# Kernel optimization log

Measured on AMD Instinct MI355X. Metric: run time of the kernel, lower is better.

The kernel has to match this reference:

```python
import jax, jax.numpy as jnp
import numpy as np

EPS = 1e-9


def setup_inputs() -> dict:
    key = jax.random.key(0)
    kE, kQ, kK, kV = jax.random.split(key, 4)
    B, S, D = 8, 2048, 256
    return {
        "E": jax.random.normal(kE, (B, S, D), dtype=jnp.float32),
        "WQ": jax.random.normal(kQ, (D, D), dtype=jnp.float32) * (1.0 / np.sqrt(D)),
        "WK": jax.random.normal(kK, (D, D), dtype=jnp.float32) * (1.0 / np.sqrt(D)),
        "WV": jax.random.normal(kV, (D, D), dtype=jnp.float32) * (1.0 / np.sqrt(D)),
    }


def reference(E, WQ, WK, WV):
    # E: [B, S, D]; WQ/WK/WV: [D, D] (torch Linear weight, applied as x @ W.T)
    D = E.shape[-1]
    scale = jnp.asarray(np.sqrt(D), dtype=E.dtype)
    Q = jnp.einsum('bsd,ed->bse', E, WQ)
    K = jnp.einsum('bsd,ed->bse', E, WK)
    V = jnp.einsum('bsd,ed->bse', E, WV)
    # Full score matrix [B, S, S] (non-flash, as in the original)
    W = jnp.einsum('bqd,bkd->bqk', Q, K) / scale
    # mask=True path: causal tril mask, additionally zeroed where W == 0 exactly
    S_len = W.shape[-1]
    tril = jnp.tril(jnp.ones((S_len, S_len), dtype=W.dtype))  # [S, S]
    M = jnp.where(W == 0, jnp.zeros_like(W), tril[None, :, :])
    # custom masked softmax with epsilon denominator
    x_max = jnp.max(W, axis=-1, keepdims=True)
    x_exp = jnp.exp(W - x_max) * M
    A = x_exp / (jnp.sum(x_exp, axis=-1, keepdims=True) + EPS)
    return jnp.einsum('bqk,bkd->bqd', A, V)
```

## Files before the change

kernel.cpp:

```cpp
#include <hip/hip_runtime.h>
#include <hip/hip_bf16.h>
#include <stdint.h>


typedef __attribute__((ext_vector_type(8)))  short bf16x8;
typedef __attribute__((ext_vector_type(4)))  float f32x4;
typedef __attribute__((ext_vector_type(16))) float f32x16;
typedef __attribute__((ext_vector_type(4)))  unsigned int u32x4;

#define NEGF  -3.0e38f
#define MINIT -1.0e30f

__device__ __forceinline__ unsigned short f2bf(float f){
  union { float f; unsigned u; } v; v.f = f;
  unsigned r = v.u + 0x7FFFu + ((v.u >> 16) & 1u);
  return (unsigned short)(r >> 16);
}
__device__ __forceinline__ unsigned pk2(float a, float b){
  return (unsigned)f2bf(a) | ((unsigned)f2bf(b) << 16);
}
__device__ __forceinline__ unsigned short f2bf_n(float f){
  __hip_bfloat16 h = __float2bfloat16(f);
  return *reinterpret_cast<unsigned short*>(&h);
}
__device__ __forceinline__ unsigned pk2_n(float a, float b){
  return (unsigned)f2bf_n(a) | ((unsigned)f2bf_n(b) << 16);
}
__device__ __forceinline__ float bf2f(unsigned short h){
  union { unsigned u; float f; } v; v.u = ((unsigned)h) << 16; return v.f;
}

__global__ void wconv_kernel(const float* __restrict__ WQ, const float* __restrict__ WK,
                             const float* __restrict__ WV, unsigned short* __restrict__ Wb)
{
  const int widx = blockIdx.x, kk = blockIdx.y, n = threadIdx.x;
  const float* W = (widx==0) ? WQ : ((widx==1) ? WK : WV);
  unsigned short* dst = Wb + (size_t)widx*65536 + kk*8192 + n*32;
#pragma unroll
  for (int gp=0; gp<4; ++gp){
    const int g = gp ^ (n & 3);
    const float* src = W + (size_t)n*256 + kk*32 + g*8;
    float4 a = *reinterpret_cast<const float4*>(src);
    float4 c = *reinterpret_cast<const float4*>(src + 4);
    uint4 v; v.x = pk2(a.x,a.y); v.y = pk2(a.z,a.w); v.z = pk2(c.x,c.y); v.w = pk2(c.z,c.w);
    *reinterpret_cast<uint4*>(dst + gp*8) = v;
  }
}

__global__ __launch_bounds__(256, 3) void qkv_proj_kernel(
    const float* __restrict__ E, const unsigned short* __restrict__ Wb,
    unsigned short* __restrict__ Qb, unsigned short* __restrict__ Ka,
    unsigned short* __restrict__ Vf)
{
  __shared__ unsigned short As[32*256];
  __shared__ unsigned short Bs[2][8192];

  const int m0 = blockIdx.x * 32;
  const int b  = m0 >> 11;
  const int sb = m0 & 2047;
  const int t = threadIdx.x, lane = t & 63, w = t >> 6;
  const int hi = lane >> 4, lo = lane & 15;

  auto stageB = [&](int widx, int kk, int buf){
    const char* src = (const char*)Wb + widx*131072 + kk*16384;
    char* dst = (char*)Bs[buf];
#pragma unroll
    for (int c=0;c<4;c++){
      const int off = c*4096 + t*16;
      __builtin_amdgcn_global_load_lds(
        (const __attribute__((address_space(1))) unsigned int*)(src + off),
        (__attribute__((address_space(3))) unsigned int*)(dst + off), 16, 0, 0);
    }
  };

  stageB(0, 0, 0);
  {
    const int r = t >> 3, c0 = (t & 7) * 32;
    const float* ga = E + (size_t)(m0 + r)*256 + c0;
#pragma unroll
    for (int gg=0; gg<4; ++gg){
      float4 x = *reinterpret_cast<const float4*>(ga + gg*8);
      float4 y = *reinterpret_cast<const float4*>(ga + gg*8 + 4);
      uint4 v; v.x = pk2(x.x,x.y); v.y = pk2(x.z,x.w); v.z = pk2(y.x,y.y); v.w = pk2(y.z,y.w);
      const int g = (t & 7)*4 + gg;
      *reinterpret_cast<uint4*>((char*)As + r*512 + ((g ^ (r & 7)) << 4)) = v;
    }
  }

  const f32x4 fzero = {0.f,0.f,0.f,0.f};
  const int u = sb >> 5;
  for (int widx=0; widx<3; ++widx){
    f32x4 acc[2][4];
#pragma unroll
    for (int mi=0;mi<2;mi++)
#pragma unroll
      for (int f=0;f<4;f++) acc[mi][f] = fzero;
    if (widx) stageB(widx, 0, 0);

    for (int kk=0; kk<8; ++kk){
      const int bb = kk & 1;
      if (kk < 7) stageB(widx, kk+1, bb^1);
      if (kk < 7) asm volatile("s_waitcnt vmcnt(4) lgkmcnt(0)" ::: "memory");
      else        asm volatile("s_waitcnt vmcnt(0) lgkmcnt(0)" ::: "memory");
      __builtin_amdgcn_sched_barrier(0);
      __builtin_amdgcn_s_barrier();
      __builtin_amdgcn_sched_barrier(0);

      bf16x8 afr[2], bfr[4];
#pragma unroll
      for (int mi=0;mi<2;mi++){
        const int r = mi*16 + lo;
        afr[mi] = *reinterpret_cast<const bf16x8*>(
            (const char*)As + r*512 + (((kk*4 + hi) ^ (r & 7)) << 4));
      }
#pragma unroll
      for (int f=0;f<4;f++){
        const int n = w*64 + f*16 + lo;
        bfr[f] = *reinterpret_cast<const bf16x8*>(
            (const char*)Bs[bb] + n*64 + ((hi ^ (n & 3)) << 4));
      }
#pragma unroll
      for (int mi=0;mi<2;mi++)
#pragma unroll
        for (int f=0;f<4;f++)
          acc[mi][f] = __builtin_amdgcn_mfma_f32_16x16x32_bf16(afr[mi], bfr[f], acc[mi][f], 0,0,0);

      asm volatile("s_waitcnt lgkmcnt(0)" ::: "memory");
      __builtin_amdgcn_sched_barrier(0);
      __builtin_amdgcn_s_barrier();
    }

    if (widx == 0){
#pragma unroll
      for (int mi=0;mi<2;mi++)
#pragma unroll
        for (int f=0;f<4;f++){
          const int col = w*64 + f*16 + lo;
#pragma unroll
          for (int r=0;r<4;r++)
            Qb[(size_t)(m0 + mi*16 + hi*4 + r)*256 + col] = f2bf(acc[mi][f][r]*0.0625f);
        }
    } else if (widx == 1){
      unsigned short* Kab = Ka + (size_t)b*524288 + (size_t)u*8192;
#pragma unroll
      for (int mi=0;mi<2;mi++)
#pragma unroll
        for (int f=0;f<4;f++){
          const int c = w*4 + f;
          const int j = lo & 7;
          const int lb = 32*(lo>>3) + mi*16 + hi*4;
#pragma unroll
          for (int r=0;r<4;r++)
            Kab[(size_t)(c*64 + lb + r)*8 + j] = f2bf(acc[mi][f][r]);
        }
    } else {
      unsigned short* Vfb = Vf + (size_t)b*524288;
#pragma unroll
      for (int mi=0;mi<2;mi++)
#pragma unroll
        for (int f=0;f<4;f++){
          const int d  = w*64 + f*16 + lo;
          const int dt = d >> 5;
          const int l  = 32*(hi&1) + (d&31);
          const int j0 = 4*(hi>>1);
          unsigned short* vp = Vfb + ((size_t)((u*2 + mi)*8 + dt)*64 + l)*8 + j0;
          uint2 pw; pw.x = pk2(acc[mi][f][0], acc[mi][f][1]);
          pw.y = pk2(acc[mi][f][2], acc[mi][f][3]);
          *reinterpret_cast<uint2*>(vp) = pw;
        }
    }
  }
}

__global__ __launch_bounds__(256, 2) void attn_kernel(
    const unsigned short* __restrict__ Qb, const unsigned short* __restrict__ Ka,
    const unsigned short* __restrict__ Vf, float* __restrict__ Out,
    const int sched, unsigned short* __restrict__ Pb, float* __restrict__ ML)
{
  __shared__ char Lds[2][32768];

  const int bid  = blockIdx.x;
  const int b    = bid & 7;
  const int slot = bid >> 3;
  int tau, chunk, mode, u0, u1;
  if (sched){
    const int ts = slot >> 1; chunk = slot & 1;
    tau = (ts < 16) ? (31 - ts) : (ts - 16);
    u0 = chunk ? (tau + 1) : 0;
    u1 = chunk ? (2*tau + 2) : (tau + 1);
    mode = 1 + chunk;
  } else {
    tau = 31 - slot; chunk = 0; u0 = 0; u1 = 2*tau + 2; mode = 0;
  }
  const int Qbase = tau * 64;

  const int t = threadIdx.x;
  const int lane = t & 63, w = t >> 6;
  const int qs = w >> 1, dh = w & 1;
  const int l31 = lane & 31, h5 = lane >> 5;
  const int q_l = Qbase + qs*32 + l31;
  const int diagu = 2*tau + qs;

  const char* Kab = (const char*)Ka + (size_t)b*1048576;
  const char* Vfb = (const char*)Vf + (size_t)b*1048576;

  auto stage = [&](int uu, int buf){
    const char* gk = Kab + (size_t)uu*16384;
    const char* gv = Vfb + (size_t)uu*16384;
    char* lk = Lds[buf];
    char* lv = Lds[buf] + 16384;
#pragma unroll
    for (int i=0;i<4;i++){
      const int off = i*4096 + t*16;
      __builtin_amdgcn_global_load_lds(
        (const __attribute__((address_space(1))) unsigned int*)(gk + off),
        (__attribute__((address_space(3))) unsigned int*)(lk + off), 16, 0, 0);
      __builtin_amdgcn_global_load_lds(
        (const __attribute__((address_space(1))) unsigned int*)(gv + off),
        (__attribute__((address_space(3))) unsigned int*)(lv + off), 16, 0, 0);
    }
  };

  bf16x8 qf[16];
  {
    const unsigned short* Qp = Qb + ((size_t)(b*2048 + q_l))*256 + h5*8;
#pragma unroll
    for (int c=0;c<16;c++) qf[c] = *reinterpret_cast<const bf16x8*>(Qp + c*16);
  }

  const f32x16 z16 = {0.f,0.f,0.f,0.f,0.f,0.f,0.f,0.f,0.f,0.f,0.f,0.f,0.f,0.f,0.f,0.f};
  f32x16 accO[4];
#pragma unroll
  for (int i=0;i<4;i++) accO[i] = z16;
  float m_run = MINIT, l_run = 0.f;

  stage(u0, 0);
  if (u0 + 1 < u1) stage(u0 + 1, 1);

  for (int u = u0; u < u1; ++u){
    const int buf = (u - u0) & 1;
    if (u + 1 < u1) asm volatile("s_waitcnt vmcnt(8)" ::: "memory");
    else            asm volatile("s_waitcnt vmcnt(0)" ::: "memory");
    __builtin_amdgcn_sched_barrier(0);
    __builtin_amdgcn_s_barrier();
    __builtin_amdgcn_sched_barrier(0);

    const char* kt = Lds[buf];
    const char* lv = Lds[buf] + 16384 + dh*4096 + lane*16;

    f32x16 sv0 = z16, sv1 = z16;
#pragma unroll
    for (int c=0;c<16;c+=2){
      bf16x8 a0 = *reinterpret_cast<const bf16x8*>(kt + c*1024 + lane*16);
      bf16x8 a1 = *reinterpret_cast<const bf16x8*>(kt + (c+1)*1024 + lane*16);
      sv0 = __builtin_amdgcn_mfma_f32_32x32x16_bf16(a0, qf[c],   sv0, 0,0,0);
      sv1 = __builtin_amdgcn_mfma_f32_32x32x16_bf16(a1, qf[c+1], sv1, 0,0,0);
    }
    f32x16 s16 = sv0 + sv1;

    bf16x8 vf0[4], vf1[4];
#pragma unroll
    for (int i=0;i<4;i++){
      vf0[i] = *reinterpret_cast<const bf16x8*>(lv + i*1024);
      vf1[i] = *reinterpret_cast<const bf16x8*>(lv + 8192 + i*1024);
    }

    if (u >= diagu){
      const int kvb = u*32 + 4*h5;
#pragma unroll
      for (int r=0;r<16;r++){
        const int kv = kvb + (r&3) + 8*(r>>2);
        if (kv > q_l) s16[r] = NEGF;
      }
    }

    float t8[8], t4[4];
#pragma unroll
    for (int i=0;i<8;i++) t8[i] = fmaxf(s16[i], s16[i+8]);
#pragma unroll
    for (int i=0;i<4;i++) t4[i] = fmaxf(t8[i], t8[i+4]);
    float pmax = fmaxf(fmaxf(t4[0],t4[1]), fmaxf(t4[2],t4[3]));
    pmax = fmaxf(pmax, __shfl_xor(pmax, 32, 64));

    if (!__all(pmax - m_run <= 8.0f)){
      const float mn = fmaxf(m_run, pmax);
      const float alpha = __expf(m_run - mn);
#pragma unroll
      for (int i=0;i<4;i++) accO[i] *= alpha;
      l_run *= alpha;
      m_run = mn;
    }
    float p[16];
#pragma unroll
    for (int r=0;r<16;r++) p[r] = __expf(s16[r] - m_run);
#pragma unroll
    for (int i=0;i<8;i++) t8[i] = p[i] + p[i+8];
#pragma unroll
    for (int i=0;i<4;i++) t4[i] = t8[i] + t8[i+4];
    float ls = (t4[0]+t4[1]) + (t4[2]+t4[3]);
    ls += __shfl_xor(ls, 32, 64);
    l_run += ls;

    union { bf16x8 v; unsigned u32[4]; } pa0, pa1;
#pragma unroll
    for (int k=0;k<4;k++){
      pa0.u32[k] = pk2_n(p[2*k],   p[2*k+1]);
      pa1.u32[k] = pk2_n(p[8+2*k], p[9+2*k]);
    }

#pragma unroll
    for (int i=0;i<4;i++){
      accO[i] = __builtin_amdgcn_mfma_f32_32x32x16_bf16(vf0[i], pa0.v, accO[i], 0,0,0);
      accO[i] = __builtin_amdgcn_mfma_f32_32x32x16_bf16(vf1[i], pa1.v, accO[i], 0,0,0);
    }

    asm volatile("s_waitcnt lgkmcnt(0)" ::: "memory");
    __builtin_amdgcn_sched_barrier(0);
    __builtin_amdgcn_s_barrier();
    if (u + 2 < u1) stage(u + 2, buf);
  }

  if (mode && dh == 0 && lane < 32){
    float* mlp = ML + ((size_t)(((b*32 + tau)*2 + chunk)*64 + qs*32 + lane))*2;
    mlp[0] = m_run; mlp[1] = l_run;
  }

  const float inv = (mode == 0) ? 1.0f/(l_run + 1e-9f) : 1.0f;
  float* Tw = (float*)(&Lds[0][0]) + w*2048;
  const int qloc = lane >> 1, dc = (lane & 1) * 16;
#pragma unroll
  for (int i=0;i<4;i++){
#pragma unroll
    for (int r=0;r<16;r++)
      Tw[l31*33 + ((r&3) + 8*(r>>2) + 4*h5)] = accO[i][r] * inv;
    asm volatile("s_waitcnt lgkmcnt(0)" ::: "memory");
    __builtin_amdgcn_sched_barrier(0);
    const float* srcT = &Tw[qloc*33 + dc];
    if (mode < 2){
      float* dst = Out + ((size_t)(b*2048 + Qbase + qs*32 + qloc))*256 + dh*128 + i*32 + dc;
#pragma unroll
      for (int k=0;k<4;k++){
        float4 vv = { srcT[4*k], srcT[4*k+1], srcT[4*k+2], srcT[4*k+3] };
        *reinterpret_cast<float4*>(dst + 4*k) = vv;
      }
    } else {
      unsigned short* pb = Pb + (((size_t)(b*32 + tau)*64 + qs*32 + qloc))*256
                              + dh*128 + i*32 + dc;
      u32x4 w0, w1;
      w0.x = pk2_n(srcT[0],  srcT[1]);  w0.y = pk2_n(srcT[2],  srcT[3]);
      w0.z = pk2_n(srcT[4],  srcT[5]);  w0.w = pk2_n(srcT[6],  srcT[7]);
      w1.x = pk2_n(srcT[8],  srcT[9]);  w1.y = pk2_n(srcT[10], srcT[11]);
      w1.z = pk2_n(srcT[12], srcT[13]); w1.w = pk2_n(srcT[14], srcT[15]);
      *reinterpret_cast<u32x4*>(pb)     = w0;
      *reinterpret_cast<u32x4*>(pb + 8) = w1;
    }
    asm volatile("s_waitcnt lgkmcnt(0)" ::: "memory");
    __builtin_amdgcn_sched_barrier(0);
  }
}

__global__ void combine_kernel(float* __restrict__ Out, const unsigned short* __restrict__ Pb,
                               const float* __restrict__ ML)
{
  const int b = blockIdx.x & 7, tt = blockIdx.x >> 3;
  const int t = threadIdx.x;
  const int q = t >> 2, dg = (t & 3) * 64;
  const float* mlp = ML + ((size_t)((b*32 + tt)*2)*64)*2;
  const float m0 = mlp[q*2],        l0 = mlp[q*2 + 1];
  const float m1 = mlp[(64+q)*2],   l1 = mlp[(64+q)*2 + 1];
  const float M  = fmaxf(m0, m1);
  const float e0 = __expf(m0 - M), e1 = __expf(m1 - M);
  const float inv = 1.0f/(e0*l0 + e1*l1 + 1e-9f);
  float* O = Out + ((size_t)(b*2048 + tt*64 + q))*256 + dg;
  const unsigned short* P = Pb + ((size_t)((b*32 + tt)*64 + q))*256 + dg;
#pragma unroll
  for (int k=0;k<8;k++){
    float4 a0 = *reinterpret_cast<const float4*>(O + 8*k);
    float4 a1 = *reinterpret_cast<const float4*>(O + 8*k + 4);
    uint4 pvv = *reinterpret_cast<const uint4*>(P + 8*k);
    const unsigned short* us = (const unsigned short*)&pvv;
    float4 o0, o1;
    o0.x = (e0*a0.x + e1*bf2f(us[0]))*inv; o0.y = (e0*a0.y + e1*bf2f(us[1]))*inv;
    o0.z = (e0*a0.z + e1*bf2f(us[2]))*inv; o0.w = (e0*a0.w + e1*bf2f(us[3]))*inv;
    o1.x = (e0*a1.x + e1*bf2f(us[4]))*inv; o1.y = (e0*a1.y + e1*bf2f(us[5]))*inv;
    o1.z = (e0*a1.z + e1*bf2f(us[6]))*inv; o1.w = (e0*a1.w + e1*bf2f(us[7]))*inv;
    *reinterpret_cast<float4*>(O + 8*k)     = o0;
    *reinterpret_cast<float4*>(O + 8*k + 4) = o1;
  }
}

extern "C" void kernel_launch(void* const* d_in, const int* in_sizes, int n_in,
                              void* d_out, int out_size, void* d_ws, size_t ws_size,
                              hipStream_t stream)
{
  const float* E  = (const float*)d_in[0];
  const float* WQ = (const float*)d_in[1];
  const float* WK = (const float*)d_in[2];
  const float* WV = (const float*)d_in[3];
  const size_t elems = (size_t)8*2048*256;

  unsigned short* Qb = (unsigned short*)d_ws;
  unsigned short* Ka = Qb + elems;
  unsigned short* Vf = Ka + elems;
  unsigned short* Wb = Vf + elems;
  const size_t base = 3*elems*2 + 393216;

  const size_t PB = (size_t)8*32*64*256*2;
  const size_t MLSZ = (size_t)8*32*2*64*2*4;
  if (ws_size < base) return;
  const int sched = (ws_size >= base + PB + MLSZ) ? 1 : 0;
  unsigned short* Pb = (unsigned short*)((char*)d_ws + base);
  float* ML = (float*)((char*)d_ws + base + PB);

  wconv_kernel<<<dim3(3,8), 256, 0, stream>>>(WQ, WK, WV, Wb);
  qkv_proj_kernel<<<512, 256, 0, stream>>>(E, Wb, Qb, Ka, Vf);
  attn_kernel<<<sched ? 512 : 256, 256, 0, stream>>>(Qb, Ka, Vf, (float*)d_out, sched, Pb, ML);
  if (sched) combine_kernel<<<256, 256, 0, stream>>>((float*)d_out, Pb, ML);
}
```

Measured before the change: 85.66 us.

## Split long causal query tiles into four KV chunks with generalized combine

Adds a third schedule where query tiles with tau>=20 are split into four KV chunks instead of two, raising the attention grid to 704 blocks for better load balance across CUs. The combine kernel is generalized to merge up to four partial results using stored max/sum pairs. It also widens the QK^T MFMA accumulation to four independent chains to expose more ILP. The cost is more partial-output traffic in bf16 and a larger workspace requirement; if the workspace is too small the old schedule is used.

```diff
diff --git a/kernel.cpp b/kernel.cpp
--- a/kernel.cpp
+++ b/kernel.cpp
@@ -28,6 +28,18 @@
 }
 __device__ __forceinline__ float bf2f(unsigned short h){
   union { unsigned u; float f; } v; v.u = ((unsigned)h) << 16; return v.f;
+}
+
+__device__ __host__ __forceinline__ int nch_of(int tau, int sched){
+  return (sched == 2 && tau >= 20) ? 4 : 2;
+}
+__device__ __forceinline__ int pbase_of(int tau, int sched){
+  if (sched == 2) return (tau <= 20) ? tau : 20 + (tau - 20)*3;
+  return tau;
+}
+__device__ __forceinline__ int mlbase_of(int tau, int sched){
+  if (sched == 2) return (tau <= 20) ? 2*tau : 40 + (tau - 20)*4;
+  return 2*tau;
 }
 
 __global__ void wconv_kernel(const float* __restrict__ WQ, const float* __restrict__ WK,
@@ -175,7 +187,8 @@
 __global__ __launch_bounds__(256, 2) void attn_kernel(
     const unsigned short* __restrict__ Qb, const unsigned short* __restrict__ Ka,
     const unsigned short* __restrict__ Vf, float* __restrict__ Out,
-    const int sched, unsigned short* __restrict__ Pb, float* __restrict__ ML)
+    const int sched, unsigned short* __restrict__ Pb, float* __restrict__ ML,
+    const int psl, const int mls)
 {
   __shared__ char Lds[2][32768];
 
@@ -183,7 +196,17 @@
   const int b    = bid & 7;
   const int slot = bid >> 3;
   int tau, chunk, mode, u0, u1;
-  if (sched){
+  if (sched == 2){
+    int nch;
+    if (slot < 8)       { tau = 19 - (slot >> 1); chunk = slot & 1;      nch = 2; }
+    else if (slot < 56) { int s = slot - 8;  tau = 31 - (s >> 2); chunk = s & 3; nch = 4; }
+    else                { int s = slot - 56; tau = 15 - (s >> 1); chunk = s & 1; nch = 2; }
+    const int len = 2*tau + 2;
+    const int qq = len / nch, rem = len - qq*nch;
+    u0 = chunk*qq + ((chunk < rem) ? chunk : rem);
+    u1 = u0 + qq + ((chunk < rem) ? 1 : 0);
+    mode = (chunk == 0) ? 1 : 2;
+  } else if (sched == 1){
     const int ts = slot >> 1; chunk = slot & 1;
     tau = (ts < 16) ? (31 - ts) : (ts - 16);
     u0 = chunk ? (tau + 1) : 0;
@@ -248,15 +271,19 @@
     const char* kt = Lds[buf];
     const char* lv = Lds[buf] + 16384 + dh*4096 + lane*16;
 
-    f32x16 sv0 = z16, sv1 = z16;
-#pragma unroll
-    for (int c=0;c<16;c+=2){
+    f32x16 sv0 = z16, sv1 = z16, sv2 = z16, sv3 = z16;
+#pragma unroll
+    for (int c=0;c<16;c+=4){
       bf16x8 a0 = *reinterpret_cast<const bf16x8*>(kt + c*1024 + lane*16);
       bf16x8 a1 = *reinterpret_cast<const bf16x8*>(kt + (c+1)*1024 + lane*16);
+      bf16x8 a2 = *reinterpret_cast<const bf16x8*>(kt + (c+2)*1024 + lane*16);
+      bf16x8 a3 = *reinterpret_cast<const bf16x8*>(kt + (c+3)*1024 + lane*16);
       sv0 = __builtin_amdgcn_mfma_f32_32x32x16_bf16(a0, qf[c],   sv0, 0,0,0);
       sv1 = __builtin_amdgcn_mfma_f32_32x32x16_bf16(a1, qf[c+1], sv1, 0,0,0);
-    }
-    f32x16 s16 = sv0 + sv1;
+      sv2 = __builtin_amdgcn_mfma_f32_32x32x16_bf16(a2, qf[c+2], sv2, 0,0,0);
+      sv3 = __builtin_amdgcn_mfma_f32_32x32x16_bf16(a3, qf[c+3], sv3, 0,0,0);
+    }
+    f32x16 s16 = (sv0 + sv1) + (sv2 + sv3);
 
     bf16x8 vf0[4], vf1[4];
 #pragma unroll
@@ -321,7 +348,7 @@
   }
 
   if (mode && dh == 0 && lane < 32){
-    float* mlp = ML + ((size_t)(((b*32 + tau)*2 + chunk)*64 + qs*32 + lane))*2;
+    float* mlp = ML + ((size_t)(b*mls + mlbase_of(tau, sched) + chunk)*64 + qs*32 + lane)*2;
     mlp[0] = m_run; mlp[1] = l_run;
   }
 
@@ -344,7 +371,7 @@
         *reinterpret_cast<float4*>(dst + 4*k) = vv;
       }
     } else {
-      unsigned short* pb = Pb + (((size_t)(b*32 + tau)*64 + qs*32 + qloc))*256
+      unsigned short* pb = Pb + ((size_t)(b*psl + pbase_of(tau, sched) + (chunk-1))*64 + qs*32 + qloc)*256
                               + dh*128 + i*32 + dc;
       u32x4 w0, w1;
       w0.x = pk2_n(srcT[0],  srcT[1]);  w0.y = pk2_n(srcT[2],  srcT[3]);
@@ -360,32 +387,56 @@
 }
 
 __global__ void combine_kernel(float* __restrict__ Out, const unsigned short* __restrict__ Pb,
-                               const float* __restrict__ ML)
+                               const float* __restrict__ ML, const int sched,
+                               const int psl, const int mls)
 {
   const int b = blockIdx.x & 7, tt = blockIdx.x >> 3;
+  const int nch = nch_of(tt, sched);
+  const int pbase = (sched == 2) ? ((tt <= 20) ? tt : 20 + (tt - 20)*3) : tt;
+  const int mlbase = (sched == 2) ? ((tt <= 20) ? 2*tt : 40 + (tt - 20)*4) : 2*tt;
   const int t = threadIdx.x;
   const int q = t >> 2, dg = (t & 3) * 64;
-  const float* mlp = ML + ((size_t)((b*32 + tt)*2)*64)*2;
-  const float m0 = mlp[q*2],        l0 = mlp[q*2 + 1];
-  const float m1 = mlp[(64+q)*2],   l1 = mlp[(64+q)*2 + 1];
-  const float M  = fmaxf(m0, m1);
-  const float e0 = __expf(m0 - M), e1 = __expf(m1 - M);
-  const float inv = 1.0f/(e0*l0 + e1*l1 + 1e-9f);
+
+  float mc[4], lc[4];
+#pragma unroll
+  for (int c=0;c<4;c++){
+    if (c < nch){
+      const float* mlp = ML + ((size_t)(b*mls + mlbase + c)*64 + q)*2;
+      mc[c] = mlp[0]; lc[c] = mlp[1];
+    } else { mc[c] = MINIT; lc[c] = 0.f; }
+  }
+  float M = fmaxf(fmaxf(mc[0],mc[1]), fmaxf(mc[2],mc[3]));
+  float e[4], L = 0.f;
+#pragma unroll
+  for (int c=0;c<4;c++){ e[c] = __expf(mc[c] - M); L += e[c]*lc[c]; }
+  const float inv = 1.0f/(L + 1e-9f);
+
   float* O = Out + ((size_t)(b*2048 + tt*64 + q))*256 + dg;
-  const unsigned short* P = Pb + ((size_t)((b*32 + tt)*64 + q))*256 + dg;
-#pragma unroll
-  for (int k=0;k<8;k++){
-    float4 a0 = *reinterpret_cast<const float4*>(O + 8*k);
-    float4 a1 = *reinterpret_cast<const float4*>(O + 8*k + 4);
-    uint4 pvv = *reinterpret_cast<const uint4*>(P + 8*k);
-    const unsigned short* us = (const unsigned short*)&pvv;
-    float4 o0, o1;
-    o0.x = (e0*a0.x + e1*bf2f(us[0]))*inv; o0.y = (e0*a0.y + e1*bf2f(us[1]))*inv;
-    o0.z = (e0*a0.z + e1*bf2f(us[2]))*inv; o0.w = (e0*a0.w + e1*bf2f(us[3]))*inv;
-    o1.x = (e0*a1.x + e1*bf2f(us[4]))*inv; o1.y = (e0*a1.y + e1*bf2f(us[5]))*inv;
-    o1.z = (e0*a1.z + e1*bf2f(us[6]))*inv; o1.w = (e0*a1.w + e1*bf2f(us[7]))*inv;
-    *reinterpret_cast<float4*>(O + 8*k)     = o0;
-    *reinterpret_cast<float4*>(O + 8*k + 4) = o1;
+  f32x4 acc[16];
+#pragma unroll
+  for (int k=0;k<16;k++){
+    f32x4 v = *reinterpret_cast<const f32x4*>(O + 4*k);
+    acc[k] = v * e[0];
+  }
+#pragma unroll
+  for (int c=1;c<4;c++){
+    if (c < nch){
+      const unsigned short* P = Pb + ((size_t)(b*psl + pbase + (c-1))*64 + q)*256 + dg;
+#pragma unroll
+      for (int k=0;k<8;k++){
+        u32x4 pv = *reinterpret_cast<const u32x4*>(P + 8*k);
+        const unsigned short* us = (const unsigned short*)&pv;
+#pragma unroll
+        for (int j=0;j<4;j++) acc[2*k][j]   += e[c]*bf2f(us[j]);
+#pragma unroll
+        for (int j=0;j<4;j++) acc[2*k+1][j] += e[c]*bf2f(us[4+j]);
+      }
+    }
+  }
+#pragma unroll
+  for (int k=0;k<16;k++){
+    f32x4 v = acc[k] * inv;
+    *reinterpret_cast<f32x4*>(O + 4*k) = v;
   }
 }
 
@@ -405,15 +456,17 @@
   unsigned short* Wb = Vf + elems;
   const size_t base = 3*elems*2 + 393216;
 
-  const size_t PB = (size_t)8*32*64*256*2;
-  const size_t MLSZ = (size_t)8*32*2*64*2*4;
+  const size_t PB2 = (size_t)8*56*64*256*2, ML2 = (size_t)8*88*64*2*4;
+  const size_t PB1 = (size_t)8*32*64*256*2, ML1 = (size_t)8*64*64*2*4;
   if (ws_size < base) return;
-  const int sched = (ws_size >= base + PB + MLSZ) ? 1 : 0;
+  int sched = 0, psl = 0, mls = 0, grid = 256;
+  if (ws_size >= base + PB2 + ML2){ sched = 2; psl = 56; mls = 88; grid = 704; }
+  else if (ws_size >= base + PB1 + ML1){ sched = 1; psl = 32; mls = 64; grid = 512; }
   unsigned short* Pb = (unsigned short*)((char*)d_ws + base);
-  float* ML = (float*)((char*)d_ws + base + PB);
+  float* ML = (float*)((char*)d_ws + base + ((sched == 2) ? PB2 : PB1));
 
   wconv_kernel<<<dim3(3,8), 256, 0, stream>>>(WQ, WK, WV, Wb);
   qkv_proj_kernel<<<512, 256, 0, stream>>>(E, Wb, Qb, Ka, Vf);
-  attn_kernel<<<sched ? 512 : 256, 256, 0, stream>>>(Qb, Ka, Vf, (float*)d_out, sched, Pb, ML);
-  if (sched) combine_kernel<<<256, 256, 0, stream>>>((float*)d_out, Pb, ML);
-}
+  attn_kernel<<<grid, 256, 0, stream>>>(Qb, Ka, Vf, (float*)d_out, sched, Pb, ML, psl, mls);
+  if (sched) combine_kernel<<<256, 256, 0, stream>>>((float*)d_out, Pb, ML, sched, psl, mls);
+}
```

After: 92.03 us. 1.07x slower.

## Load V fragments directly from global into registers and halve LDS staging

Applied to the files above, without the earlier changes.

The attention kernel now stages only K tiles through LDS and loads each wave's V fragments straight from global memory into registers at the top of every iteration. The barrier and next-tile prefetch move to right after the QK MFMAs, so the buffer refill overlaps with the softmax. A vmcnt wait is placed before the PV MFMAs. This halves LDS use per block, which could allow more occupancy, and removes one LDS round trip for V. In exchange, V fetches now sit on the per-iteration critical path, served from L2 or global memory. Separately, the manual round-to-nearest bf16 conversion is replaced by the library __float2bfloat16 in the projection kernels.

```diff
diff --git a/kernel.cpp b/kernel.cpp
--- a/kernel.cpp
+++ b/kernel.cpp
@@ -11,14 +11,6 @@
 #define NEGF  -3.0e38f
 #define MINIT -1.0e30f
 
-__device__ __forceinline__ unsigned short f2bf(float f){
-  union { float f; unsigned u; } v; v.f = f;
-  unsigned r = v.u + 0x7FFFu + ((v.u >> 16) & 1u);
-  return (unsigned short)(r >> 16);
-}
-__device__ __forceinline__ unsigned pk2(float a, float b){
-  return (unsigned)f2bf(a) | ((unsigned)f2bf(b) << 16);
-}
 __device__ __forceinline__ unsigned short f2bf_n(float f){
   __hip_bfloat16 h = __float2bfloat16(f);
   return *reinterpret_cast<unsigned short*>(&h);
@@ -42,7 +34,7 @@
     const float* src = W + (size_t)n*256 + kk*32 + g*8;
     float4 a = *reinterpret_cast<const float4*>(src);
     float4 c = *reinterpret_cast<const float4*>(src + 4);
-    uint4 v; v.x = pk2(a.x,a.y); v.y = pk2(a.z,a.w); v.z = pk2(c.x,c.y); v.w = pk2(c.z,c.w);
+    uint4 v; v.x = pk2_n(a.x,a.y); v.y = pk2_n(a.z,a.w); v.z = pk2_n(c.x,c.y); v.w = pk2_n(c.z,c.w);
     *reinterpret_cast<uint4*>(dst + gp*8) = v;
   }
 }
@@ -81,7 +73,7 @@
     for (int gg=0; gg<4; ++gg){
       float4 x = *reinterpret_cast<const float4*>(ga + gg*8);
       float4 y = *reinterpret_cast<const float4*>(ga + gg*8 + 4);
-      uint4 v; v.x = pk2(x.x,x.y); v.y = pk2(x.z,x.w); v.z = pk2(y.x,y.y); v.w = pk2(y.z,y.w);
+      uint4 v; v.x = pk2_n(x.x,x.y); v.y = pk2_n(x.z,x.w); v.z = pk2_n(y.x,y.y); v.w = pk2_n(y.z,y.w);
       const int g = (t & 7)*4 + gg;
       *reinterpret_cast<uint4*>((char*)As + r*512 + ((g ^ (r & 7)) << 4)) = v;
     }
@@ -138,7 +130,7 @@
           const int col = w*64 + f*16 + lo;
 #pragma unroll
           for (int r=0;r<4;r++)
-            Qb[(size_t)(m0 + mi*16 + hi*4 + r)*256 + col] = f2bf(acc[mi][f][r]*0.0625f);
+            Qb[(size_t)(m0 + mi*16 + hi*4 + r)*256 + col] = f2bf_n(acc[mi][f][r]*0.0625f);
         }
     } else if (widx == 1){
       unsigned short* Kab = Ka + (size_t)b*524288 + (size_t)u*8192;
@@ -151,7 +143,7 @@
           const int lb = 32*(lo>>3) + mi*16 + hi*4;
 #pragma unroll
           for (int r=0;r<4;r++)
-            Kab[(size_t)(c*64 + lb + r)*8 + j] = f2bf(acc[mi][f][r]);
+            Kab[(size_t)(c*64 + lb + r)*8 + j] = f2bf_n(acc[mi][f][r]);
         }
     } else {
       unsigned short* Vfb = Vf + (size_t)b*524288;
@@ -164,8 +156,8 @@
           const int l  = 32*(hi&1) + (d&31);
           const int j0 = 4*(hi>>1);
           unsigned short* vp = Vfb + ((size_t)((u*2 + mi)*8 + dt)*64 + l)*8 + j0;
-          uint2 pw; pw.x = pk2(acc[mi][f][0], acc[mi][f][1]);
-          pw.y = pk2(acc[mi][f][2], acc[mi][f][3]);
+          uint2 pw; pw.x = pk2_n(acc[mi][f][0], acc[mi][f][1]);
+          pw.y = pk2_n(acc[mi][f][2], acc[mi][f][3]);
           *reinterpret_cast<uint2*>(vp) = pw;
         }
     }
@@ -177,7 +169,7 @@
     const unsigned short* __restrict__ Vf, float* __restrict__ Out,
     const int sched, unsigned short* __restrict__ Pb, float* __restrict__ ML)
 {
-  __shared__ char Lds[2][32768];
+  __shared__ char Kt[2][16384];
 
   const int bid  = blockIdx.x;
   const int b    = bid & 7;
@@ -206,18 +198,13 @@
 
   auto stage = [&](int uu, int buf){
     const char* gk = Kab + (size_t)uu*16384;
-    const char* gv = Vfb + (size_t)uu*16384;
-    char* lk = Lds[buf];
-    char* lv = Lds[buf] + 16384;
+    char* lk = Kt[buf];
 #pragma unroll
     for (int i=0;i<4;i++){
       const int off = i*4096 + t*16;
       __builtin_amdgcn_global_load_lds(
         (const __attribute__((address_space(1))) unsigned int*)(gk + off),
         (__attribute__((address_space(3))) unsigned int*)(lk + off), 16, 0, 0);
-      __builtin_amdgcn_global_load_lds(
-        (const __attribute__((address_space(1))) unsigned int*)(gv + off),
-        (__attribute__((address_space(3))) unsigned int*)(lv + off), 16, 0, 0);
     }
   };
 
@@ -239,15 +226,22 @@
 
   for (int u = u0; u < u1; ++u){
     const int buf = (u - u0) & 1;
-    if (u + 1 < u1) asm volatile("s_waitcnt vmcnt(8)" ::: "memory");
+    if (u + 1 < u1) asm volatile("s_waitcnt vmcnt(4)" ::: "memory");
     else            asm volatile("s_waitcnt vmcnt(0)" ::: "memory");
     __builtin_amdgcn_sched_barrier(0);
     __builtin_amdgcn_s_barrier();
     __builtin_amdgcn_sched_barrier(0);
 
-    const char* kt = Lds[buf];
-    const char* lv = Lds[buf] + 16384 + dh*4096 + lane*16;
-
+    const char* Vu = Vfb + (size_t)u*16384 + dh*4096 + lane*16;
+    bf16x8 vf0[4], vf1[4];
+#pragma unroll
+    for (int i=0;i<4;i++){
+      vf0[i] = *reinterpret_cast<const bf16x8*>(Vu + i*1024);
+      vf1[i] = *reinterpret_cast<const bf16x8*>(Vu + 8192 + i*1024);
+    }
+    __builtin_amdgcn_sched_barrier(0);
+
+    const char* kt = Kt[buf];
     f32x16 sv0 = z16, sv1 = z16;
 #pragma unroll
     for (int c=0;c<16;c+=2){
@@ -258,12 +252,11 @@
     }
     f32x16 s16 = sv0 + sv1;
 
-    bf16x8 vf0[4], vf1[4];
-#pragma unroll
-    for (int i=0;i<4;i++){
-      vf0[i] = *reinterpret_cast<const bf16x8*>(lv + i*1024);
-      vf1[i] = *reinterpret_cast<const bf16x8*>(lv + 8192 + i*1024);
-    }
+    asm volatile("s_waitcnt lgkmcnt(0)" ::: "memory");
+    __builtin_amdgcn_sched_barrier(0);
+    __builtin_amdgcn_s_barrier();
+    if (u + 2 < u1) stage(u + 2, buf);
+    __builtin_amdgcn_sched_barrier(0);
 
     if (u >= diagu){
       const int kvb = u*32 + 4*h5;
@@ -308,16 +301,15 @@
       pa1.u32[k] = pk2_n(p[8+2*k], p[9+2*k]);
     }
 
+    if (u + 2 < u1) asm volatile("s_waitcnt vmcnt(4)" ::: "memory");
+    else            asm volatile("s_waitcnt vmcnt(0)" ::: "memory");
+    __builtin_amdgcn_sched_barrier(0);
+
 #pragma unroll
     for (int i=0;i<4;i++){
       accO[i] = __builtin_amdgcn_mfma_f32_32x32x16_bf16(vf0[i], pa0.v, accO[i], 0,0,0);
       accO[i] = __builtin_amdgcn_mfma_f32_32x32x16_bf16(vf1[i], pa1.v, accO[i], 0,0,0);
     }
-
-    asm volatile("s_waitcnt lgkmcnt(0)" ::: "memory");
-    __builtin_amdgcn_sched_barrier(0);
-    __builtin_amdgcn_s_barrier();
-    if (u + 2 < u1) stage(u + 2, buf);
   }
 
   if (mode && dh == 0 && lane < 32){
@@ -326,7 +318,7 @@
   }
 
   const float inv = (mode == 0) ? 1.0f/(l_run + 1e-9f) : 1.0f;
-  float* Tw = (float*)(&Lds[0][0]) + w*2048;
+  float* Tw = (float*)(&Kt[0][0]) + w*2048;
   const int qloc = lane >> 1, dc = (lane & 1) * 16;
 #pragma unroll
   for (int i=0;i<4;i++){
```

Result: slower. 96.54 us (+12.7%).
